# Performance work log

Hardware: AMD Instinct MI355X
Metric: run time of the kernel (lower is better)

The kernel has to match this reference:

```python
import jax, jax.numpy as jnp
import numpy as np

H = 16        # num_heads
E = 1024      # embed_size
OUT = 1024    # out_dim
TEMP = 1.0
EPS = 1e-20
LN_EPS = 1e-5


def setup_inputs() -> dict:
    key = jax.random.key(0)
    ks = jax.random.split(key, 16)
    B, S = 8, 4096
    s = 1.0 / np.sqrt(E)
    inp = {
        'x': jax.random.normal(ks[0], (B, S, E), dtype=jnp.float32),
        'gumbel_u': jax.random.uniform(ks[1], (B, H, S, 2), dtype=jnp.float32, minval=1e-6, maxval=1.0 - 1e-6),
        'query': jax.random.uniform(ks[2], (1, E), dtype=jnp.float32, minval=-s, maxval=s),  # xavier-ish
        'Wq': jax.random.uniform(ks[3], (E, E), jnp.float32, -s, s),
        'bq': jnp.zeros((E,), jnp.float32),
        'Wk': jax.random.uniform(ks[4], (E, E), jnp.float32, -s, s),
        'bk': jnp.zeros((E,), jnp.float32),
        'Wv': jax.random.uniform(ks[5], (E, E), jnp.float32, -s, s),
        'bv': jnp.zeros((E,), jnp.float32),
        'ln_g': jnp.ones((E,), jnp.float32),
        'ln_b': jnp.zeros((E,), jnp.float32),
        'W1': jax.random.uniform(ks[6], (4 * E, E), jnp.float32, -s, s),
        'b1': jnp.zeros((4 * E,), jnp.float32),
        'W2': jax.random.uniform(ks[7], (OUT, 4 * E), jnp.float32, -0.5 * s, 0.5 * s),
        'b2': jnp.zeros((OUT,), jnp.float32),
    }
    return inp


def reference(x, gumbel_u, query, Wq, bq, Wk, bk, Wv, bv, ln_g, ln_b, W1, b1, W2, b2):
    B, S, _ = x.shape
    dk = E // H
    # projections
    q = (query @ Wq.T + bq).reshape(H, dk)                      # [H, dk] (single query, broadcast over batch)
    k = (x @ Wk.T + bk).reshape(B, S, H, dk)                    # [B, S, H, dk]
    v = (x @ Wv.T + bv).reshape(B, S, H, dk)
    # single-query attention logits
    logits = jnp.einsum('hd,bshd->bhs', q, k) / np.sqrt(dk)     # [B, H, S]
    probs = jax.nn.softmax(logits, axis=-1)                     # [B, H, S]
    # gumbel-softmax hard mask over {keep=0-logit, drop/keep pair}
    edges = jnp.stack([jnp.zeros_like(logits), logits], axis=-1)  # [B, H, S, 2]
    g = -jnp.log(-jnp.log(gumbel_u + EPS) + EPS)
    y_soft = jax.nn.softmax((edges + g) / TEMP, axis=-1)
    idx = jnp.argmax(y_soft, axis=-1)
    y_hard = jax.nn.one_hot(idx, 2, dtype=y_soft.dtype)
    y = jax.lax.stop_gradient(y_hard - y_soft) + y_soft         # straight-through
    A = y[..., 1]                                               # [B, H, S]
    probs = A * probs
    # weighted sum of values; merge heads (seq_len of query is 1)
    hidden = jnp.einsum('bhs,bshd->bhd', probs, v).reshape(B, E)
    # layernorm
    mu = hidden.mean(axis=-1, keepdims=True)
    var = hidden.var(axis=-1, keepdims=True)
    hidden = (hidden - mu) / jnp.sqrt(var + LN_EPS) * ln_g + ln_b
    # MLP (dropout p=0 -> identity)
    out = jax.nn.relu(hidden @ W1.T + b1) @ W2.T + b2           # [B, OUT]
    masks = A.sum(axis=1)[:, None, :]                           # sum_heads=True -> [B, 1, S]
    attn = probs.sum(axis=1)[:, None, :]
    return out, masks, attn
```

## Files before the change

### kernel.cpp

```cpp
#include <hip/hip_runtime.h>
#include <hip/hip_bf16.h>
#include <math.h>

#define SS 4096
#define EE 1024
#define HH 16

typedef __bf16 bf16x8 __attribute__((ext_vector_type(8)));
typedef float  f32x4v __attribute__((ext_vector_type(4)));

#define OFF_QVEC 0L
#define OFF_QKB  1024L
#define OFF_QH   1040L
#define OFF_QL   9232L
#define OFF_SEC  17424L
#define OFF_SAC  50192L
#define OFF_WG   82960L
#define OFF_HID  607248L
#define OFF_T1   615440L
#define OFF_PX   648208L

__device__ __forceinline__ unsigned int pk_hi(float a, float b){
  return __builtin_amdgcn_perm(__float_as_uint(b), __float_as_uint(a), 0x07060302u);
}
__device__ __forceinline__ float lo_part(float f){
  return f - __uint_as_float(__float_as_uint(f) & 0xFFFF0000u);
}
__device__ __forceinline__ unsigned short f2bf_rn(float f){
  unsigned int u = __float_as_uint(f);
  return (unsigned short)((u + 0x7fffu + ((u >> 16) & 1u)) >> 16);
}
__device__ __forceinline__ f32x4v mfma16(bf16x8 a, bf16x8 b, f32x4v c){
  return __builtin_amdgcn_mfma_f32_16x16x32_bf16(a, b, c, 0, 0, 0);
}
__device__ __forceinline__ float waveRedSum(float v){
  #pragma unroll
  for (int m=1;m<64;m<<=1) v += __shfl_xor(v, m, 64);
  return v;
}
template<int NW>
__device__ __forceinline__ float blockRedSum(float v, volatile float* scr){
  v = waveRedSum(v);
  const int w = threadIdx.x >> 6;
  __syncthreads();
  if ((threadIdx.x & 63) == 0) scr[w] = v;
  __syncthreads();
  float r = 0.f;
  #pragma unroll
  for (int i=0;i<NW;i++) r += scr[i];
  return r;
}

__global__ __launch_bounds__(256) void k1(const float* __restrict__ query, const float* __restrict__ Wq,
                                          const float* __restrict__ bq, float* __restrict__ qvec,
                                          float* __restrict__ hid){
  const int wv = threadIdx.x >> 6, lane = threadIdx.x & 63;
  const int j = blockIdx.x * 4 + wv;
  float p = 0.f;
  #pragma unroll
  for (int i=0;i<4;i++){
    const int e = 4*lane + 256*i;
    const float4 q4 = *(const float4*)(query + e);
    const float4 w4 = *(const float4*)(Wq + (long)j*EE + e);
    p += q4.x*w4.x + q4.y*w4.y + q4.z*w4.z + q4.w*w4.w;
  }
  p = waveRedSum(p);
  if (lane == 0) qvec[j] = p + bq[j];
  if (blockIdx.x < 32) hid[blockIdx.x*256 + threadIdx.x] = 0.f;
}

__global__ __launch_bounds__(256) void k2(const float* __restrict__ Wk, const float* __restrict__ bk,
                                          const float* __restrict__ qvec,
                                          unsigned short* __restrict__ qh, unsigned short* __restrict__ ql,
                                          float* __restrict__ qkb){
  __shared__ float red[4][64];
  const int wv = threadIdx.x >> 6, lane = threadIdx.x & 63;
  const int h = blockIdx.y;
  const int e = blockIdx.x*64 + lane;
  float acc = 0.f;
  #pragma unroll
  for (int dd=0; dd<16; dd++){
    const int d = wv*16 + dd;
    acc += qvec[h*64+d] * Wk[(long)(h*64+d)*EE + e];
  }
  red[wv][lane] = acc;
  __syncthreads();
  if (wv == 0){
    const float s = red[0][lane] + red[1][lane] + red[2][lane] + red[3][lane];
    const unsigned int ub = __float_as_uint(s);
    qh[h*EE + e] = (unsigned short)(ub >> 16);
    const float lo = s - __uint_as_float(ub & 0xFFFF0000u);
    ql[h*EE + e] = (unsigned short)(__float_as_uint(lo) >> 16);
    if (blockIdx.x == 0){
      float p = qvec[h*64+lane] * bk[h*64+lane];
      p = waveRedSum(p);
      if (lane == 0) qkb[h] = p;
    }
  }
}

__global__ __launch_bounds__(256,2) void k3f(const float* __restrict__ x, const float* __restrict__ gum,
                                             const unsigned short* __restrict__ qh, const unsigned short* __restrict__ ql,
                                             const float* __restrict__ qkb,
                                             float* __restrict__ seC, float* __restrict__ saC,
                                             float* __restrict__ Wg, float* __restrict__ px,
                                             float* __restrict__ out){
  __shared__ unsigned short xsT[4][256*32];
  __shared__ float lg[4*16*17];
  __shared__ float wT[16][20];
  __shared__ float scrA[16*17], scrB[16*17];
  __shared__ float sQkb[16];
  const int t = threadIdx.x;
  const int wv = t >> 6, lane = t & 63;
  const int m16 = lane & 15, q = lane >> 4;
  const int blk = blockIdx.x, b = blockIdx.y;
  if (t < 16) sQkb[t] = qkb[t];
  unsigned short* xw = &xsT[wv][0];

  f32x4v P[16];
  #pragma unroll
  for (int i=0;i<16;i++){ P[i][0]=0.f; P[i][1]=0.f; P[i][2]=0.f; P[i][3]=0.f; }

  for (int ch=0; ch<4; ch++){
    const int c = blk*4 + ch;
    const long xbase = ((long)(b*SS + c*16))*EE;

    f32x4v a = {0.f,0.f,0.f,0.f};
    #pragma unroll
    for (int kt=0; kt<8; kt++){
      const int k = wv*256 + kt*32 + q*8;
      const float* xp = x + xbase + (long)m16*EE + k;
      const float4 f0 = *(const float4*)(xp);
      const float4 f1 = *(const float4*)(xp + 4);
      union { uint4 u; bf16x8 v; } xh, xl, bh, bl;
      xh.u.x = pk_hi(f0.x, f0.y); xh.u.y = pk_hi(f0.z, f0.w);
      xh.u.z = pk_hi(f1.x, f1.y); xh.u.w = pk_hi(f1.z, f1.w);
      xl.u.x = pk_hi(lo_part(f0.x), lo_part(f0.y)); xl.u.y = pk_hi(lo_part(f0.z), lo_part(f0.w));
      xl.u.z = pk_hi(lo_part(f1.x), lo_part(f1.y)); xl.u.w = pk_hi(lo_part(f1.z), lo_part(f1.w));
      bh.u = *(const uint4*)(qh + (long)m16*EE + k);
      bl.u = *(const uint4*)(ql + (long)m16*EE + k);
      a = mfma16(xh.v, bh.v, a);
      a = mfma16(xh.v, bl.v, a);
      a = mfma16(xl.v, bh.v, a);
      const int e0 = kt*32 + q*8;
      const unsigned hw[4] = {xh.u.x, xh.u.y, xh.u.z, xh.u.w};
      const unsigned lw[4] = {xl.u.x, xl.u.y, xl.u.z, xl.u.w};
      #pragma unroll
      for (int jj=0; jj<8; jj++){
        const unsigned sh = (jj & 1) * 16;
        xw[(e0+jj)*32 + m16]      = (unsigned short)(hw[jj>>1] >> sh);
        xw[(e0+jj)*32 + 16 + m16] = (unsigned short)(lw[jj>>1] >> sh);
      }
    }
    #pragma unroll
    for (int r=0;r<4;r++)
      lg[(wv*16 + q*4 + r)*17 + m16] = a[r];
    __syncthreads();

    {
      const int h = t & 15, s = t >> 4;
      const float dot = lg[(0*16+s)*17+h] + lg[(1*16+s)*17+h]
                      + lg[(2*16+s)*17+h] + lg[(3*16+s)*17+h];
      const float logit = (dot + sQkb[h]) * 0.125f;
      const long gi = ((long)(b*16 + h))*SS + c*16 + s;
      const float2 g2 = *(const float2*)(gum + 2*gi);
      const double gg0 = -log(-log((double)g2.x + 1e-20) + 1e-20);
      const double gg1 = -log(-log((double)g2.y + 1e-20) + 1e-20);
      const float e = expf(logit);
      const float wval = ((double)logit + gg1 > gg0) ? e : 0.f;
      wT[h][s] = wval;
      Wg[((long)b*SS + c*16 + s)*16 + h] = wval;
      scrA[s*17 + h] = e;
      scrB[s*17 + h] = wval;
    }
    __syncthreads();

    if (t < 16){
      float S = 0.f, SA = 0.f, cnt = 0.f;
      #pragma unroll
      for (int i=0;i<16;i++){ S += scrA[i*17 + t]; SA += scrB[i*17 + t]; }
      #pragma unroll
      for (int hh=0; hh<16; hh++) cnt += (scrB[t*17 + hh] > 0.f) ? 1.f : 0.f;
      seC[((long)(b*16 + t))*256 + c] = S;
      saC[((long)(b*16 + t))*256 + c] = SA;
      out[8192 + (long)b*SS + c*16 + t] = cnt;
    }

    {
      float wf[8];
      *(float4*)&wf[0] = *(const float4*)&wT[m16][(q & 1)*8];
      *(float4*)&wf[4] = *(const float4*)&wT[m16][(q & 1)*8 + 4];
      union { uint4 u; bf16x8 v; } B1, B2;
      B1.u.x = pk_hi(wf[0],wf[1]); B1.u.y = pk_hi(wf[2],wf[3]);
      B1.u.z = pk_hi(wf[4],wf[5]); B1.u.w = pk_hi(wf[6],wf[7]);
      B2.u.x = pk_hi(lo_part(wf[0]),lo_part(wf[1])); B2.u.y = pk_hi(lo_part(wf[2]),lo_part(wf[3]));
      B2.u.z = pk_hi(lo_part(wf[4]),lo_part(wf[5])); B2.u.w = pk_hi(lo_part(wf[6]),lo_part(wf[7]));
      #pragma unroll
      for (int et=0; et<16; et++){
        union { uint4 u; bf16x8 v; } A;
        A.u = *(const uint4*)(xw + (et*16 + m16)*32 + q*8);
        P[et] = mfma16(A.v, B1.v, P[et]);
        P[et] = mfma16(A.v, B2.v, P[et]);
      }
    }
  }

  const long pbase = (((long)(b*64 + blk))*16 + m16)*1024 + wv*256;
  #pragma unroll
  for (int et=0; et<16; et++){
    #pragma unroll
    for (int r=0;r<4;r++)
      px[pbase + et*16 + q*4 + r] = P[et][r];
  }
}

__global__ __launch_bounds__(256) void kb(const float* __restrict__ px, const float* __restrict__ Wg,
                                          const float* __restrict__ seC, const float* __restrict__ saC,
                                          const float* __restrict__ Wv, const float* __restrict__ bv,
                                          float* __restrict__ hid, float* __restrict__ out){
  __shared__ float s_red[16][17];
  __shared__ float sInv[16];
  __shared__ float scr1[4], scr2[4];
  __shared__ float xs[256];
  const int t = threadIdx.x;

  if (blockIdx.x < 32){
    const int b = blockIdx.x >> 2, sq = blockIdx.x & 3;
    { const int h = t >> 4, cl = t & 15;
      float se = 0.f;
      #pragma unroll
      for (int k=0;k<16;k++) se += seC[((long)(b*16+h))*256 + cl + 16*k];
      s_red[h][cl] = se;
    }
    __syncthreads();
    if (t < 16){
      float D = 0.f;
      #pragma unroll
      for (int i=0;i<16;i++) D += s_red[t][i];
      sInv[t] = 1.f / D;
    }
    __syncthreads();
    #pragma unroll
    for (int it=0; it<4; it++){
      const int s = sq*1024 + it*256 + t;
      const float* wr = Wg + ((long)b*SS + s)*16;
      float a = 0.f;
      #pragma unroll
      for (int h=0;h<16;h++) a += wr[h]*sInv[h];
      out[40960 + (long)b*SS + s] = a;
    }
    return;
  }

  const int idx = blockIdx.x - 32;
  const int b = idx >> 6, h = (idx >> 2) & 15, eq = idx & 3;
  const long rbase = ((long)(b*16 + h))*256;
  const float D    = blockRedSum<4>(seC[rbase + t], scr1);
  const float SA   = blockRedSum<4>(saC[rbase + t], scr2);
  const float invD = 1.f / D;
  const float psum = SA * invD;
  const float* pp = px + (((long)(b*64))*16 + h)*1024 + eq*256 + t;
  float xa = 0.f;
  #pragma unroll 8
  for (int seg=0; seg<64; seg++) xa += pp[(long)seg*16384];
  xs[t] = xa;
  __syncthreads();
  const int wv = t >> 6, lane = t & 63;
  const float4 xv = *(const float4*)(xs + 4*lane);
  #pragma unroll 4
  for (int jj=0; jj<16; jj++){
    const int j = h*64 + wv*16 + jj;
    const float4 w4 = *(const float4*)(Wv + (long)j*EE + eq*256 + 4*lane);
    float p = xv.x*w4.x + xv.y*w4.y + xv.z*w4.z + xv.w*w4.w;
    p = waveRedSum(p);
    if (lane == 0){
      float add = p * invD;
      if (eq == 0) add += psum * bv[j];
      atomicAdd(&hid[(long)b*EE + j], add);
    }
  }
}

__global__ __launch_bounds__(256) void k8f(const float* __restrict__ hid, const float* __restrict__ lng,
                                           const float* __restrict__ lnb, const float* __restrict__ W1,
                                           const float* __restrict__ b1, const float* __restrict__ b2,
                                           unsigned short* __restrict__ t1u, float* __restrict__ out){
  __shared__ unsigned short h2[16*1032];
  __shared__ float red[4*64*4];
  const int t = threadIdx.x;
  if (blockIdx.x < 32) out[blockIdx.x*256 + t] = b2[(blockIdx.x & 3)*256 + t];

  {
    const int r = t >> 5, ll = t & 31;
    float4 vv[8];
    float s1 = 0.f, s2 = 0.f;
    #pragma unroll
    for (int i=0;i<8;i++){
      vv[i] = *(const float4*)(hid + (long)r*1024 + ll*32 + i*4);
      s1 += vv[i].x + vv[i].y + vv[i].z + vv[i].w;
      s2 += vv[i].x*vv[i].x + vv[i].y*vv[i].y + vv[i].z*vv[i].z + vv[i].w*vv[i].w;
    }
    #pragma unroll
    for (int m=1;m<32;m<<=1){ s1 += __shfl_xor(s1, m, 32); s2 += __shfl_xor(s2, m, 32); }
    const float mu  = s1 * (1.f/1024.f);
    const float var = s2 * (1.f/1024.f) - mu*mu;
    const float rs  = rsqrtf(var + 1e-5f);
    #pragma unroll
    for (int i=0;i<8;i++){
      const int e = ll*32 + i*4;
      const float4 g4 = *(const float4*)(lng + e);
      const float4 b4 = *(const float4*)(lnb + e);
      uint2 pk;
      pk.x = (unsigned)f2bf_rn((vv[i].x-mu)*rs*g4.x + b4.x) | ((unsigned)f2bf_rn((vv[i].y-mu)*rs*g4.y + b4.y) << 16);
      pk.y = (unsigned)f2bf_rn((vv[i].z-mu)*rs*g4.z + b4.z) | ((unsigned)f2bf_rn((vv[i].w-mu)*rs*g4.w + b4.w) << 16);
      *(uint2*)(h2 + r*1032 + e) = pk;
      *(uint2*)(h2 + (8+r)*1032 + e) = make_uint2(0u, 0u);
    }
  }
  __syncthreads();

  const int wv = t >> 6, lane = t & 63;
  const int m16 = lane & 15, q = lane >> 4;
  const int j = blockIdx.x*16 + m16;
  f32x4v a = {0.f,0.f,0.f,0.f};
  #pragma unroll
  for (int kt=0; kt<8; kt++){
    const int k = wv*256 + kt*32 + q*8;
    union { uint4 u; bf16x8 v; } A, B;
    A.u = *(const uint4*)(h2 + m16*1032 + k);
    const float4 f0 = *(const float4*)(W1 + (long)j*EE + k);
    const float4 f1 = *(const float4*)(W1 + (long)j*EE + k + 4);
    B.u.x = pk_hi(f0.x,f0.y); B.u.y = pk_hi(f0.z,f0.w);
    B.u.z = pk_hi(f1.x,f1.y); B.u.w = pk_hi(f1.z,f1.w);
    a = mfma16(A.v, B.v, a);
  }
  #pragma unroll
  for (int r=0;r<4;r++) red[(wv*64 + lane)*4 + r] = a[r];
  __syncthreads();
  if (wv == 0){
    #pragma unroll
    for (int r=0;r<4;r++){
      const float s = red[(0*64+lane)*4+r] + red[(1*64+lane)*4+r]
                    + red[(2*64+lane)*4+r] + red[(3*64+lane)*4+r];
      const int row = q*4 + r;
      const float val = (row < 8) ? fmaxf(s + b1[j], 0.f) : 0.f;
      t1u[(long)row*4096 + j] = f2bf_rn(val);
    }
  }
}

__global__ __launch_bounds__(256) void k9a(const unsigned short* __restrict__ t1u, const float* __restrict__ W2,
                                           float* __restrict__ out){
  __shared__ float red[4*64*4];
  const int wv = threadIdx.x >> 6, lane = threadIdx.x & 63;
  const int m16 = lane & 15, q = lane >> 4;
  const int o = blockIdx.x*16 + m16;
  const int kbase = blockIdx.y*1024 + wv*256;
  f32x4v a = {0.f,0.f,0.f,0.f};
  #pragma unroll
  for (int kt=0; kt<8; kt++){
    const int k = kbase + kt*32 + q*8;
    union { uint4 u; bf16x8 v; } A, B;
    A.u = *(const uint4*)(t1u + (long)m16*4096 + k);
    const float4 f0 = *(const float4*)(W2 + (long)o*4096 + k);
    const float4 f1 = *(const float4*)(W2 + (long)o*4096 + k + 4);
    B.u.x = pk_hi(f0.x,f0.y); B.u.y = pk_hi(f0.z,f0.w);
    B.u.z = pk_hi(f1.x,f1.y); B.u.w = pk_hi(f1.z,f1.w);
    a = mfma16(A.v, B.v, a);
  }
  #pragma unroll
  for (int r=0;r<4;r++) red[(wv*64 + lane)*4 + r] = a[r];
  __syncthreads();
  if (wv == 0){
    #pragma unroll
    for (int r=0;r<4;r++){
      const int row = q*4 + r;
      if (row < 8){
        const float s = red[(0*64+lane)*4+r] + red[(1*64+lane)*4+r]
                      + red[(2*64+lane)*4+r] + red[(3*64+lane)*4+r];
        atomicAdd(out + row*1024 + o, s);
      }
    }
  }
}

extern "C" void kernel_launch(void* const* d_in, const int* in_sizes, int n_in,
                              void* d_out, int out_size, void* d_ws, size_t ws_size,
                              hipStream_t stream){
  const float* x    = (const float*)d_in[0];
  const float* gum  = (const float*)d_in[1];
  const float* query= (const float*)d_in[2];
  const float* Wq   = (const float*)d_in[3];
  const float* bq   = (const float*)d_in[4];
  const float* Wk   = (const float*)d_in[5];
  const float* bk   = (const float*)d_in[6];
  const float* Wv   = (const float*)d_in[7];
  const float* bv   = (const float*)d_in[8];
  const float* lng  = (const float*)d_in[9];
  const float* lnb  = (const float*)d_in[10];
  const float* W1   = (const float*)d_in[11];
  const float* b1   = (const float*)d_in[12];
  const float* W2   = (const float*)d_in[13];
  const float* b2   = (const float*)d_in[14];
  float* ws = (float*)d_ws;
  float* qvec = ws + OFF_QVEC;
  float* qkb  = ws + OFF_QKB;
  unsigned short* qh = (unsigned short*)(ws + OFF_QH);
  unsigned short* ql = (unsigned short*)(ws + OFF_QL);
  float* seC  = ws + OFF_SEC;
  float* saC  = ws + OFF_SAC;
  float* Wg   = ws + OFF_WG;
  float* hid  = ws + OFF_HID;
  unsigned short* t1u = (unsigned short*)(ws + OFF_T1);
  float* px   = ws + OFF_PX;
  float* out = (float*)d_out;

  k1  <<<256, 256, 0, stream>>>(query, Wq, bq, qvec, hid);
  k2  <<<dim3(16,16), 256, 0, stream>>>(Wk, bk, qvec, qh, ql, qkb);
  k3f <<<dim3(64,8), 256, 0, stream>>>(x, gum, qh, ql, qkb, seC, saC, Wg, px, out);
  kb  <<<544, 256, 0, stream>>>(px, Wg, seC, saC, Wv, bv, hid, out);
  k8f <<<256, 256, 0, stream>>>(hid, lng, lnb, W1, b1, b2, t1u, out);
  k9a <<<dim3(64,4), 256, 0, stream>>>(t1u, W2, out);
}
```

Baseline: 292.9 us.

## Fuse pipeline into cooperative persistent kernel with grid syncs and bf16 partials

Replaces six separate kernel launches with one cooperative kernel of 512 blocks whose phases are separated by grid-wide syncs, and keeps a multi-launch fallback. Idle blocks in the early phases precompute the double-precision Gumbel threshold differences, which takes the log work out of the attention phase. The per-block value partials are stored in bf16 instead of fp32 to halve that traffic, and the work split of the final GEMV and the attention-output pass is rebalanced. The risks are grid-sync overhead, lower occupancy from the large shared-memory footprint, and a small accuracy loss from bf16 partial sums.

```diff
diff --git a/kernel.cpp b/kernel.cpp
--- a/kernel.cpp
+++ b/kernel.cpp
@@ -1,6 +1,9 @@
 #include <hip/hip_runtime.h>
 #include <hip/hip_bf16.h>
+#include <hip/hip_cooperative_groups.h>
 #include <math.h>
+
+namespace cg = cooperative_groups;
 
 #define SS 4096
 #define EE 1024
@@ -18,8 +21,22 @@
 #define OFF_WG   82960L
 #define OFF_HID  607248L
 #define OFF_T1   615440L
-#define OFF_PX   648208L
-
+#define OFF_INVD 648208L
+#define OFF_PSUM 648336L
+#define OFF_PX   648464L
+#define OFF_GTH  4842768L
+
+struct MP {
+  const float *x, *gum, *query, *Wq, *bq, *Wk, *bk, *Wv, *bv, *lng, *lnb, *W1, *b1, *W2, *b2;
+  float *qvec, *qkb, *seC, *saC, *Wg, *hid, *invD, *psum;
+  double *gth;
+  unsigned short *qh, *ql, *t1u, *px;
+  float *out;
+};
+
+__device__ __forceinline__ float bf2f(unsigned int u){
+  union { unsigned int i; float f; } c; c.i = u << 16; return c.f;
+}
 __device__ __forceinline__ unsigned int pk_hi(float a, float b){
   return __builtin_amdgcn_perm(__float_as_uint(b), __float_as_uint(a), 0x07060302u);
 }
@@ -51,71 +68,85 @@
   return r;
 }
 
-__global__ __launch_bounds__(256) void k1(const float* __restrict__ query, const float* __restrict__ Wq,
-                                          const float* __restrict__ bq, float* __restrict__ qvec,
-                                          float* __restrict__ hid){
-  const int wv = threadIdx.x >> 6, lane = threadIdx.x & 63;
-  const int j = blockIdx.x * 4 + wv;
-  float p = 0.f;
-  #pragma unroll
-  for (int i=0;i<4;i++){
-    const int e = 4*lane + 256*i;
-    const float4 q4 = *(const float4*)(query + e);
-    const float4 w4 = *(const float4*)(Wq + (long)j*EE + e);
-    p += q4.x*w4.x + q4.y*w4.y + q4.z*w4.z + q4.w*w4.w;
-  }
-  p = waveRedSum(p);
-  if (lane == 0) qvec[j] = p + bq[j];
-  if (blockIdx.x < 32) hid[blockIdx.x*256 + threadIdx.x] = 0.f;
-}
-
-__global__ __launch_bounds__(256) void k2(const float* __restrict__ Wk, const float* __restrict__ bk,
-                                          const float* __restrict__ qvec,
-                                          unsigned short* __restrict__ qh, unsigned short* __restrict__ ql,
-                                          float* __restrict__ qkb){
-  __shared__ float red[4][64];
-  const int wv = threadIdx.x >> 6, lane = threadIdx.x & 63;
-  const int h = blockIdx.y;
-  const int e = blockIdx.x*64 + lane;
-  float acc = 0.f;
-  #pragma unroll
-  for (int dd=0; dd<16; dd++){
-    const int d = wv*16 + dd;
-    acc += qvec[h*64+d] * Wk[(long)(h*64+d)*EE + e];
-  }
-  red[wv][lane] = acc;
-  __syncthreads();
-  if (wv == 0){
-    const float s = red[0][lane] + red[1][lane] + red[2][lane] + red[3][lane];
-    const unsigned int ub = __float_as_uint(s);
-    qh[h*EE + e] = (unsigned short)(ub >> 16);
-    const float lo = s - __uint_as_float(ub & 0xFFFF0000u);
-    ql[h*EE + e] = (unsigned short)(__float_as_uint(lo) >> 16);
-    if (blockIdx.x == 0){
-      float p = qvec[h*64+lane] * bk[h*64+lane];
-      p = waveRedSum(p);
-      if (lane == 0) qkb[h] = p;
-    }
-  }
-}
-
-__global__ __launch_bounds__(256,2) void k3f(const float* __restrict__ x, const float* __restrict__ gum,
-                                             const unsigned short* __restrict__ qh, const unsigned short* __restrict__ ql,
-                                             const float* __restrict__ qkb,
-                                             float* __restrict__ seC, float* __restrict__ saC,
-                                             float* __restrict__ Wg, float* __restrict__ px,
-                                             float* __restrict__ out){
-  __shared__ unsigned short xsT[4][256*32];
-  __shared__ float lg[4*16*17];
-  __shared__ float wT[16][20];
-  __shared__ float scrA[16*17], scrB[16*17];
-  __shared__ float sQkb[16];
-  const int t = threadIdx.x;
+__device__ __forceinline__ double gdiff(float u0, float u1){
+  const double g0 = -log(-log((double)u0 + 1e-20) + 1e-20);
+  const double g1 = -log(-log((double)u1 + 1e-20) + 1e-20);
+  return g0 - g1;
+}
+__device__ __forceinline__ void ph_gth(const MP& p, long i0){
+  const float4 a4 = *(const float4*)(p.gum + 2*i0);
+  const float4 b4 = *(const float4*)(p.gum + 2*i0 + 4);
+  p.gth[i0+0] = gdiff(a4.x, a4.y);
+  p.gth[i0+1] = gdiff(a4.z, a4.w);
+  p.gth[i0+2] = gdiff(b4.x, b4.y);
+  p.gth[i0+3] = gdiff(b4.z, b4.w);
+}
+
+__device__ void phase0(const MP& p, int bid, int t){
+  const int wv = t >> 6, lane = t & 63;
+  if (bid < 256){
+    const int j = bid*4 + wv;
+    float acc = 0.f;
+    #pragma unroll
+    for (int i=0;i<4;i++){
+      const int e = 4*lane + 256*i;
+      const float4 q4 = *(const float4*)(p.query + e);
+      const float4 w4 = *(const float4*)(p.Wq + (long)j*EE + e);
+      acc += q4.x*w4.x + q4.y*w4.y + q4.z*w4.z + q4.w*w4.w;
+    }
+    acc = waveRedSum(acc);
+    if (lane == 0) p.qvec[j] = acc + p.bq[j];
+  } else {
+    const int ib = bid - 256;
+    if (ib < 32) p.hid[ib*256 + t] = 0.f;
+    else if (ib < 64) p.out[(ib-32)*256 + t] = p.b2[((ib-32)&3)*256 + t];
+    ph_gth(p, (long)ib*1024 + t*4);
+  }
+}
+
+__device__ void phase1(const MP& p, int bid, int t, char* SMc){
+  const int wv = t >> 6, lane = t & 63;
+  if (bid < 256){
+    float* red = (float*)SMc;
+    const int h = bid >> 4;
+    const int e = (bid & 15)*64 + lane;
+    float acc = 0.f;
+    #pragma unroll
+    for (int dd=0; dd<16; dd++){
+      const int d = wv*16 + dd;
+      acc += p.qvec[h*64+d] * p.Wk[(long)(h*64+d)*EE + e];
+    }
+    red[wv*64 + lane] = acc;
+    __syncthreads();
+    if (wv == 0){
+      const float s = red[lane] + red[64+lane] + red[128+lane] + red[192+lane];
+      const unsigned int ub = __float_as_uint(s);
+      p.qh[h*EE + e] = (unsigned short)(ub >> 16);
+      const float lo = s - __uint_as_float(ub & 0xFFFF0000u);
+      p.ql[h*EE + e] = (unsigned short)(__float_as_uint(lo) >> 16);
+      if ((bid & 15) == 0){
+        float pr = p.qvec[h*64+lane] * p.bk[h*64+lane];
+        pr = waveRedSum(pr);
+        if (lane == 0) p.qkb[h] = pr;
+      }
+    }
+  } else {
+    ph_gth(p, 262144L + (long)(bid-256)*1024 + t*4);
+  }
+}
+
+__device__ void phase2(const MP& p, int bid, int t, char* SMc){
+  unsigned short* xsT = (unsigned short*)SMc;
+  float* lg   = (float*)(SMc + 65536);
+  float* wT   = (float*)(SMc + 69888);
+  float* scrA = (float*)(SMc + 71168);
+  float* scrB = (float*)(SMc + 72256);
+  float* sQkb = (float*)(SMc + 73344);
   const int wv = t >> 6, lane = t & 63;
   const int m16 = lane & 15, q = lane >> 4;
-  const int blk = blockIdx.x, b = blockIdx.y;
-  if (t < 16) sQkb[t] = qkb[t];
-  unsigned short* xw = &xsT[wv][0];
+  const int blk = bid & 63, b = bid >> 6;
+  if (t < 16) sQkb[t] = p.qkb[t];
+  unsigned short* xw = xsT + wv*8192;
 
   f32x4v P[16];
   #pragma unroll
@@ -129,7 +160,7 @@
     #pragma unroll
     for (int kt=0; kt<8; kt++){
       const int k = wv*256 + kt*32 + q*8;
-      const float* xp = x + xbase + (long)m16*EE + k;
+      const float* xp = p.x + xbase + (long)m16*EE + k;
       const float4 f0 = *(const float4*)(xp);
       const float4 f1 = *(const float4*)(xp + 4);
       union { uint4 u; bf16x8 v; } xh, xl, bh, bl;
@@ -137,8 +168,8 @@
       xh.u.z = pk_hi(f1.x, f1.y); xh.u.w = pk_hi(f1.z, f1.w);
       xl.u.x = pk_hi(lo_part(f0.x), lo_part(f0.y)); xl.u.y = pk_hi(lo_part(f0.z), lo_part(f0.w));
       xl.u.z = pk_hi(lo_part(f1.x), lo_part(f1.y)); xl.u.w = pk_hi(lo_part(f1.z), lo_part(f1.w));
-      bh.u = *(const uint4*)(qh + (long)m16*EE + k);
-      bl.u = *(const uint4*)(ql + (long)m16*EE + k);
+      bh.u = *(const uint4*)(p.qh + (long)m16*EE + k);
+      bl.u = *(const uint4*)(p.ql + (long)m16*EE + k);
       a = mfma16(xh.v, bh.v, a);
       a = mfma16(xh.v, bl.v, a);
       a = mfma16(xl.v, bh.v, a);
@@ -159,17 +190,14 @@
 
     {
       const int h = t & 15, s = t >> 4;
-      const float dot = lg[(0*16+s)*17+h] + lg[(1*16+s)*17+h]
-                      + lg[(2*16+s)*17+h] + lg[(3*16+s)*17+h];
+      const float dot = lg[s*17+h] + lg[(16+s)*17+h] + lg[(32+s)*17+h] + lg[(48+s)*17+h];
       const float logit = (dot + sQkb[h]) * 0.125f;
       const long gi = ((long)(b*16 + h))*SS + c*16 + s;
-      const float2 g2 = *(const float2*)(gum + 2*gi);
-      const double gg0 = -log(-log((double)g2.x + 1e-20) + 1e-20);
-      const double gg1 = -log(-log((double)g2.y + 1e-20) + 1e-20);
+      const double gthd = p.gth[gi];
       const float e = expf(logit);
-      const float wval = ((double)logit + gg1 > gg0) ? e : 0.f;
-      wT[h][s] = wval;
-      Wg[((long)b*SS + c*16 + s)*16 + h] = wval;
+      const float wval = ((double)logit > gthd) ? e : 0.f;
+      wT[h*20 + s] = wval;
+      p.Wg[((long)b*SS + c*16 + s)*16 + h] = wval;
       scrA[s*17 + h] = e;
       scrB[s*17 + h] = wval;
     }
@@ -181,15 +209,15 @@
       for (int i=0;i<16;i++){ S += scrA[i*17 + t]; SA += scrB[i*17 + t]; }
       #pragma unroll
       for (int hh=0; hh<16; hh++) cnt += (scrB[t*17 + hh] > 0.f) ? 1.f : 0.f;
-      seC[((long)(b*16 + t))*256 + c] = S;
-      saC[((long)(b*16 + t))*256 + c] = SA;
-      out[8192 + (long)b*SS + c*16 + t] = cnt;
+      p.seC[((long)(b*16 + t))*256 + c] = S;
+      p.saC[((long)(b*16 + t))*256 + c] = SA;
+      p.out[8192 + (long)b*SS + c*16 + t] = cnt;
     }
 
     {
       float wf[8];
-      *(float4*)&wf[0] = *(const float4*)&wT[m16][(q & 1)*8];
-      *(float4*)&wf[4] = *(const float4*)&wT[m16][(q & 1)*8 + 4];
+      *(float4*)&wf[0] = *(const float4*)&wT[m16*20 + (q & 1)*8];
+      *(float4*)&wf[4] = *(const float4*)&wT[m16*20 + (q & 1)*8 + 4];
       union { uint4 u; bf16x8 v; } B1, B2;
       B1.u.x = pk_hi(wf[0],wf[1]); B1.u.y = pk_hi(wf[2],wf[3]);
       B1.u.z = pk_hi(wf[4],wf[5]); B1.u.w = pk_hi(wf[6],wf[7]);
@@ -208,61 +236,28 @@
   const long pbase = (((long)(b*64 + blk))*16 + m16)*1024 + wv*256;
   #pragma unroll
   for (int et=0; et<16; et++){
-    #pragma unroll
-    for (int r=0;r<4;r++)
-      px[pbase + et*16 + q*4 + r] = P[et][r];
-  }
-}
-
-__global__ __launch_bounds__(256) void kb(const float* __restrict__ px, const float* __restrict__ Wg,
-                                          const float* __restrict__ seC, const float* __restrict__ saC,
-                                          const float* __restrict__ Wv, const float* __restrict__ bv,
-                                          float* __restrict__ hid, float* __restrict__ out){
-  __shared__ float s_red[16][17];
-  __shared__ float sInv[16];
-  __shared__ float scr1[4], scr2[4];
-  __shared__ float xs[256];
-  const int t = threadIdx.x;
-
-  if (blockIdx.x < 32){
-    const int b = blockIdx.x >> 2, sq = blockIdx.x & 3;
-    { const int h = t >> 4, cl = t & 15;
-      float se = 0.f;
-      #pragma unroll
-      for (int k=0;k<16;k++) se += seC[((long)(b*16+h))*256 + cl + 16*k];
-      s_red[h][cl] = se;
-    }
-    __syncthreads();
-    if (t < 16){
-      float D = 0.f;
-      #pragma unroll
-      for (int i=0;i<16;i++) D += s_red[t][i];
-      sInv[t] = 1.f / D;
-    }
-    __syncthreads();
-    #pragma unroll
-    for (int it=0; it<4; it++){
-      const int s = sq*1024 + it*256 + t;
-      const float* wr = Wg + ((long)b*SS + s)*16;
-      float a = 0.f;
-      #pragma unroll
-      for (int h=0;h<16;h++) a += wr[h]*sInv[h];
-      out[40960 + (long)b*SS + s] = a;
-    }
-    return;
-  }
-
-  const int idx = blockIdx.x - 32;
-  const int b = idx >> 6, h = (idx >> 2) & 15, eq = idx & 3;
+    uint2 pk2;
+    pk2.x = (unsigned)f2bf_rn(P[et][0]) | ((unsigned)f2bf_rn(P[et][1]) << 16);
+    pk2.y = (unsigned)f2bf_rn(P[et][2]) | ((unsigned)f2bf_rn(P[et][3]) << 16);
+    *(uint2*)(p.px + pbase + et*16 + q*4) = pk2;
+  }
+}
+
+__device__ void phase3(const MP& p, int bid, int t, char* SMc){
+  float* scr1 = (float*)SMc;
+  float* scr2 = scr1 + 16;
+  float* xs   = scr1 + 32;
+  const int b = bid >> 6, h = (bid >> 2) & 15, eq = bid & 3;
   const long rbase = ((long)(b*16 + h))*256;
-  const float D    = blockRedSum<4>(seC[rbase + t], scr1);
-  const float SA   = blockRedSum<4>(saC[rbase + t], scr2);
+  const float D    = blockRedSum<4>(p.seC[rbase + t], scr1);
+  const float SA   = blockRedSum<4>(p.saC[rbase + t], scr2);
   const float invD = 1.f / D;
   const float psum = SA * invD;
-  const float* pp = px + (((long)(b*64))*16 + h)*1024 + eq*256 + t;
+  if (eq == 0 && t == 0){ p.invD[b*16+h] = invD; p.psum[b*16+h] = psum; }
+  const unsigned short* pp = p.px + (((long)(b*64))*16 + h)*1024 + eq*256 + t;
   float xa = 0.f;
   #pragma unroll 8
-  for (int seg=0; seg<64; seg++) xa += pp[(long)seg*16384];
+  for (int seg=0; seg<64; seg++) xa += bf2f((unsigned)pp[(long)seg*16384]);
   xs[t] = xa;
   __syncthreads();
   const int wv = t >> 6, lane = t & 63;
@@ -270,66 +265,107 @@
   #pragma unroll 4
   for (int jj=0; jj<16; jj++){
     const int j = h*64 + wv*16 + jj;
-    const float4 w4 = *(const float4*)(Wv + (long)j*EE + eq*256 + 4*lane);
-    float p = xv.x*w4.x + xv.y*w4.y + xv.z*w4.z + xv.w*w4.w;
-    p = waveRedSum(p);
+    const float4 w4 = *(const float4*)(p.Wv + (long)j*EE + eq*256 + 4*lane);
+    float pr = xv.x*w4.x + xv.y*w4.y + xv.z*w4.z + xv.w*w4.w;
+    pr = waveRedSum(pr);
     if (lane == 0){
-      float add = p * invD;
-      if (eq == 0) add += psum * bv[j];
-      atomicAdd(&hid[(long)b*EE + j], add);
-    }
-  }
-}
-
-__global__ __launch_bounds__(256) void k8f(const float* __restrict__ hid, const float* __restrict__ lng,
-                                           const float* __restrict__ lnb, const float* __restrict__ W1,
-                                           const float* __restrict__ b1, const float* __restrict__ b2,
-                                           unsigned short* __restrict__ t1u, float* __restrict__ out){
-  __shared__ unsigned short h2[16*1032];
-  __shared__ float red[4*64*4];
-  const int t = threadIdx.x;
-  if (blockIdx.x < 32) out[blockIdx.x*256 + t] = b2[(blockIdx.x & 3)*256 + t];
-
-  {
-    const int r = t >> 5, ll = t & 31;
-    float4 vv[8];
-    float s1 = 0.f, s2 = 0.f;
-    #pragma unroll
-    for (int i=0;i<8;i++){
-      vv[i] = *(const float4*)(hid + (long)r*1024 + ll*32 + i*4);
-      s1 += vv[i].x + vv[i].y + vv[i].z + vv[i].w;
-      s2 += vv[i].x*vv[i].x + vv[i].y*vv[i].y + vv[i].z*vv[i].z + vv[i].w*vv[i].w;
-    }
-    #pragma unroll
-    for (int m=1;m<32;m<<=1){ s1 += __shfl_xor(s1, m, 32); s2 += __shfl_xor(s2, m, 32); }
-    const float mu  = s1 * (1.f/1024.f);
-    const float var = s2 * (1.f/1024.f) - mu*mu;
-    const float rs  = rsqrtf(var + 1e-5f);
-    #pragma unroll
-    for (int i=0;i<8;i++){
-      const int e = ll*32 + i*4;
-      const float4 g4 = *(const float4*)(lng + e);
-      const float4 b4 = *(const float4*)(lnb + e);
-      uint2 pk;
-      pk.x = (unsigned)f2bf_rn((vv[i].x-mu)*rs*g4.x + b4.x) | ((unsigned)f2bf_rn((vv[i].y-mu)*rs*g4.y + b4.y) << 16);
-      pk.y = (unsigned)f2bf_rn((vv[i].z-mu)*rs*g4.z + b4.z) | ((unsigned)f2bf_rn((vv[i].w-mu)*rs*g4.w + b4.w) << 16);
-      *(uint2*)(h2 + r*1032 + e) = pk;
-      *(uint2*)(h2 + (8+r)*1032 + e) = make_uint2(0u, 0u);
-    }
-  }
-  __syncthreads();
-
+      float add = pr * invD;
+      if (eq == 0) add += psum * p.bv[j];
+      atomicAdd(&p.hid[(long)b*EE + j], add);
+    }
+  }
+}
+
+__device__ void phase4(const MP& p, int bid, int t, char* SMc){
+  const int wv = t >> 6, lane = t & 63;
+  if (bid < 256){
+    unsigned short* h2 = (unsigned short*)SMc;
+    float* red = (float*)(SMc + 33024);
+    {
+      const int r = t >> 5, ll = t & 31;
+      float4 vv[8];
+      float s1 = 0.f, s2 = 0.f;
+      #pragma unroll
+      for (int i=0;i<8;i++){
+        vv[i] = *(const float4*)(p.hid + (long)r*1024 + ll*32 + i*4);
+        s1 += vv[i].x + vv[i].y + vv[i].z + vv[i].w;
+        s2 += vv[i].x*vv[i].x + vv[i].y*vv[i].y + vv[i].z*vv[i].z + vv[i].w*vv[i].w;
+      }
+      #pragma unroll
+      for (int m=1;m<32;m<<=1){ s1 += __shfl_xor(s1, m, 32); s2 += __shfl_xor(s2, m, 32); }
+      const float mu  = s1 * (1.f/1024.f);
+      const float var = s2 * (1.f/1024.f) - mu*mu;
+      const float rs  = rsqrtf(var + 1e-5f);
+      #pragma unroll
+      for (int i=0;i<8;i++){
+        const int e = ll*32 + i*4;
+        const float4 g4 = *(const float4*)(p.lng + e);
+        const float4 b4 = *(const float4*)(p.lnb + e);
+        uint2 pk;
+        pk.x = (unsigned)f2bf_rn((vv[i].x-mu)*rs*g4.x + b4.x) | ((unsigned)f2bf_rn((vv[i].y-mu)*rs*g4.y + b4.y) << 16);
+        pk.y = (unsigned)f2bf_rn((vv[i].z-mu)*rs*g4.z + b4.z) | ((unsigned)f2bf_rn((vv[i].w-mu)*rs*g4.w + b4.w) << 16);
+        *(uint2*)(h2 + r*1032 + e) = pk;
+        *(uint2*)(h2 + (8+r)*1032 + e) = make_uint2(0u, 0u);
+      }
+    }
+    __syncthreads();
+    const int m16 = lane & 15, q = lane >> 4;
+    const int j = bid*16 + m16;
+    f32x4v a = {0.f,0.f,0.f,0.f};
+    #pragma unroll
+    for (int kt=0; kt<8; kt++){
+      const int k = wv*256 + kt*32 + q*8;
+      union { uint4 u; bf16x8 v; } A, B;
+      A.u = *(const uint4*)(h2 + m16*1032 + k);
+      const float4 f0 = *(const float4*)(p.W1 + (long)j*EE + k);
+      const float4 f1 = *(const float4*)(p.W1 + (long)j*EE + k + 4);
+      B.u.x = pk_hi(f0.x,f0.y); B.u.y = pk_hi(f0.z,f0.w);
+      B.u.z = pk_hi(f1.x,f1.y); B.u.w = pk_hi(f1.z,f1.w);
+      a = mfma16(A.v, B.v, a);
+    }
+    #pragma unroll
+    for (int r=0;r<4;r++) red[(wv*64 + lane)*4 + r] = a[r];
+    __syncthreads();
+    if (wv == 0){
+      #pragma unroll
+      for (int r=0;r<4;r++){
+        const float s = red[lane*4+r] + red[(64+lane)*4+r] + red[(128+lane)*4+r] + red[(192+lane)*4+r];
+        const int row = q*4 + r;
+        const float val = (row < 8) ? fmaxf(s + p.b1[j], 0.f) : 0.f;
+        p.t1u[(long)row*4096 + j] = f2bf_rn(val);
+      }
+    }
+  } else {
+    float* sInv = (float*)SMc;
+    const int idx2 = bid - 256;
+    const int b = idx2 >> 5, seg = idx2 & 31;
+    if (t < 16) sInv[t] = p.invD[b*16 + t];
+    __syncthreads();
+    if (t < 128){
+      const int s = seg*128 + t;
+      const float* wr = p.Wg + ((long)b*SS + s)*16;
+      float a = 0.f;
+      #pragma unroll
+      for (int h=0;h<16;h++) a += wr[h]*sInv[h];
+      p.out[40960 + (long)b*SS + s] = a;
+    }
+  }
+}
+
+__device__ void phase5(const MP& p, int bid, int t, char* SMc){
+  float* red = (float*)SMc;
   const int wv = t >> 6, lane = t & 63;
   const int m16 = lane & 15, q = lane >> 4;
-  const int j = blockIdx.x*16 + m16;
+  const int o = (bid & 63)*16 + m16;
+  const int kbase = (bid >> 6)*512 + wv*128;
   f32x4v a = {0.f,0.f,0.f,0.f};
   #pragma unroll
-  for (int kt=0; kt<8; kt++){
-    const int k = wv*256 + kt*32 + q*8;
+  for (int kt=0; kt<4; kt++){
+    const int k = kbase + kt*32 + q*8;
     union { uint4 u; bf16x8 v; } A, B;
-    A.u = *(const uint4*)(h2 + m16*1032 + k);
-    const float4 f0 = *(const float4*)(W1 + (long)j*EE + k);
-    const float4 f1 = *(const float4*)(W1 + (long)j*EE + k + 4);
+    A.u = *(const uint4*)(p.t1u + (long)m16*4096 + k);
+    const float4 f0 = *(const float4*)(p.W2 + (long)o*4096 + k);
+    const float4 f1 = *(const float4*)(p.W2 + (long)o*4096 + k + 4);
     B.u.x = pk_hi(f0.x,f0.y); B.u.y = pk_hi(f0.z,f0.w);
     B.u.z = pk_hi(f1.x,f1.y); B.u.w = pk_hi(f1.z,f1.w);
     a = mfma16(A.v, B.v, a);
@@ -340,85 +376,78 @@
   if (wv == 0){
     #pragma unroll
     for (int r=0;r<4;r++){
-      const float s = red[(0*64+lane)*4+r] + red[(1*64+lane)*4+r]
-                    + red[(2*64+lane)*4+r] + red[(3*64+lane)*4+r];
-      const int row = q*4 + r;
-      const float val = (row < 8) ? fmaxf(s + b1[j], 0.f) : 0.f;
-      t1u[(long)row*4096 + j] = f2bf_rn(val);
-    }
-  }
-}
-
-__global__ __launch_bounds__(256) void k9a(const unsigned short* __restrict__ t1u, const float* __restrict__ W2,
-                                           float* __restrict__ out){
-  __shared__ float red[4*64*4];
-  const int wv = threadIdx.x >> 6, lane = threadIdx.x & 63;
-  const int m16 = lane & 15, q = lane >> 4;
-  const int o = blockIdx.x*16 + m16;
-  const int kbase = blockIdx.y*1024 + wv*256;
-  f32x4v a = {0.f,0.f,0.f,0.f};
-  #pragma unroll
-  for (int kt=0; kt<8; kt++){
-    const int k = kbase + kt*32 + q*8;
-    union { uint4 u; bf16x8 v; } A, B;
-    A.u = *(const uint4*)(t1u + (long)m16*4096 + k);
-    const float4 f0 = *(const float4*)(W2 + (long)o*4096 + k);
-    const float4 f1 = *(const float4*)(W2 + (long)o*4096 + k + 4);
-    B.u.x = pk_hi(f0.x,f0.y); B.u.y = pk_hi(f0.z,f0.w);
-    B.u.z = pk_hi(f1.x,f1.y); B.u.w = pk_hi(f1.z,f1.w);
-    a = mfma16(A.v, B.v, a);
-  }
-  #pragma unroll
-  for (int r=0;r<4;r++) red[(wv*64 + lane)*4 + r] = a[r];
-  __syncthreads();
-  if (wv == 0){
-    #pragma unroll
-    for (int r=0;r<4;r++){
       const int row = q*4 + r;
       if (row < 8){
-        const float s = red[(0*64+lane)*4+r] + red[(1*64+lane)*4+r]
-                      + red[(2*64+lane)*4+r] + red[(3*64+lane)*4+r];
-        atomicAdd(out + row*1024 + o, s);
-      }
-    }
-  }
-}
+        const float s = red[lane*4+r] + red[(64+lane)*4+r] + red[(128+lane)*4+r] + red[(192+lane)*4+r];
+        atomicAdd(p.out + row*1024 + o, s);
+      }
+    }
+  }
+}
+
+__global__ __launch_bounds__(256,2) void mega(MP p){
+  __shared__ __align__(16) char SMc[73408];
+  cg::grid_group g = cg::this_grid();
+  const int t = threadIdx.x, bid = blockIdx.x;
+  phase0(p, bid, t);        g.sync();
+  phase1(p, bid, t, SMc);   g.sync();
+  phase2(p, bid, t, SMc);   g.sync();
+  phase3(p, bid, t, SMc);   g.sync();
+  phase4(p, bid, t, SMc);   g.sync();
+  phase5(p, bid, t, SMc);
+}
+
+__global__ __launch_bounds__(256,2) void kp0(MP p){ phase0(p, blockIdx.x, threadIdx.x); }
+__global__ __launch_bounds__(256,2) void kp1(MP p){ __shared__ __align__(16) char SMc[73408]; phase1(p, blockIdx.x, threadIdx.x, SMc); }
+__global__ __launch_bounds__(256,2) void kp2(MP p){ __shared__ __align__(16) char SMc[73408]; phase2(p, blockIdx.x, threadIdx.x, SMc); }
+__global__ __launch_bounds__(256,2) void kp3(MP p){ __shared__ __align__(16) char SMc[73408]; phase3(p, blockIdx.x, threadIdx.x, SMc); }
+__global__ __launch_bounds__(256,2) void kp4(MP p){ __shared__ __align__(16) char SMc[73408]; phase4(p, blockIdx.x, threadIdx.x, SMc); }
+__global__ __launch_bounds__(256,2) void kp5(MP p){ __shared__ __align__(16) char SMc[73408]; phase5(p, blockIdx.x, threadIdx.x, SMc); }
 
 extern "C" void kernel_launch(void* const* d_in, const int* in_sizes, int n_in,
                               void* d_out, int out_size, void* d_ws, size_t ws_size,
                               hipStream_t stream){
-  const float* x    = (const float*)d_in[0];
-  const float* gum  = (const float*)d_in[1];
-  const float* query= (const float*)d_in[2];
-  const float* Wq   = (const float*)d_in[3];
-  const float* bq   = (const float*)d_in[4];
-  const float* Wk   = (const float*)d_in[5];
-  const float* bk   = (const float*)d_in[6];
-  const float* Wv   = (const float*)d_in[7];
-  const float* bv   = (const float*)d_in[8];
-  const float* lng  = (const float*)d_in[9];
-  const float* lnb  = (const float*)d_in[10];
-  const float* W1   = (const float*)d_in[11];
-  const float* b1   = (const float*)d_in[12];
-  const float* W2   = (const float*)d_in[13];
-  const float* b2   = (const float*)d_in[14];
   float* ws = (float*)d_ws;
-  float* qvec = ws + OFF_QVEC;
-  float* qkb  = ws + OFF_QKB;
-  unsigned short* qh = (unsigned short*)(ws + OFF_QH);
-  unsigned short* ql = (unsigned short*)(ws + OFF_QL);
-  float* seC  = ws + OFF_SEC;
-  float* saC  = ws + OFF_SAC;
-  float* Wg   = ws + OFF_WG;
-  float* hid  = ws + OFF_HID;
-  unsigned short* t1u = (unsigned short*)(ws + OFF_T1);
-  float* px   = ws + OFF_PX;
-  float* out = (float*)d_out;
-
-  k1  <<<256, 256, 0, stream>>>(query, Wq, bq, qvec, hid);
-  k2  <<<dim3(16,16), 256, 0, stream>>>(Wk, bk, qvec, qh, ql, qkb);
-  k3f <<<dim3(64,8), 256, 0, stream>>>(x, gum, qh, ql, qkb, seC, saC, Wg, px, out);
-  kb  <<<544, 256, 0, stream>>>(px, Wg, seC, saC, Wv, bv, hid, out);
-  k8f <<<256, 256, 0, stream>>>(hid, lng, lnb, W1, b1, b2, t1u, out);
-  k9a <<<dim3(64,4), 256, 0, stream>>>(t1u, W2, out);
-}
+  MP p;
+  p.x    = (const float*)d_in[0];
+  p.gum  = (const float*)d_in[1];
+  p.query= (const float*)d_in[2];
+  p.Wq   = (const float*)d_in[3];
+  p.bq   = (const float*)d_in[4];
+  p.Wk   = (const float*)d_in[5];
+  p.bk   = (const float*)d_in[6];
+  p.Wv   = (const float*)d_in[7];
+  p.bv   = (const float*)d_in[8];
+  p.lng  = (const float*)d_in[9];
+  p.lnb  = (const float*)d_in[10];
+  p.W1   = (const float*)d_in[11];
+  p.b1   = (const float*)d_in[12];
+  p.W2   = (const float*)d_in[13];
+  p.b2   = (const float*)d_in[14];
+  p.qvec = ws + OFF_QVEC;
+  p.qkb  = ws + OFF_QKB;
+  p.qh   = (unsigned short*)(ws + OFF_QH);
+  p.ql   = (unsigned short*)(ws + OFF_QL);
+  p.seC  = ws + OFF_SEC;
+  p.saC  = ws + OFF_SAC;
+  p.Wg   = ws + OFF_WG;
+  p.hid  = ws + OFF_HID;
+  p.t1u  = (unsigned short*)(ws + OFF_T1);
+  p.invD = ws + OFF_INVD;
+  p.psum = ws + OFF_PSUM;
+  p.px   = (unsigned short*)(ws + OFF_PX);
+  p.gth  = (double*)(ws + OFF_GTH);
+  p.out  = (float*)d_out;
+
+  void* args[] = { (void*)&p };
+  hipError_t err = hipLaunchCooperativeKernel((const void*)mega, dim3(512), dim3(256), args, 0, stream);
+  if (err != hipSuccess){
+    (void)hipGetLastError();
+    kp0<<<512, 256, 0, stream>>>(p);
+    kp1<<<512, 256, 0, stream>>>(p);
+    kp2<<<512, 256, 0, stream>>>(p);
+    kp3<<<512, 256, 0, stream>>>(p);
+    kp4<<<512, 256, 0, stream>>>(p);
+    kp5<<<512, 256, 0, stream>>>(p);
+  }
+}
```

Result: slower. 617.4 us (+110.8%).

## Precompute gumbel thresholds in k1, pack px to bf16, repack x tile stores

Applied to the files above, without the earlier changes.

Moves the double-precision gumbel log-log computation out of the main attention kernel into extra blocks of the first kernel, which write a per-element double threshold that k3f compares against. Partial value sums px are stored as bf16 instead of fp32, halving that intermediate traffic. Shared-memory transposed x stores are merged into 32-bit writes via perm, and the output bias initialization moves to k1. This adds a B*H*S double buffer round-trip and loses precision in px.

```diff
diff --git a/kernel.cpp b/kernel.cpp
--- a/kernel.cpp
+++ b/kernel.cpp
@@ -19,7 +19,11 @@
 #define OFF_HID  607248L
 #define OFF_T1   615440L
 #define OFF_PX   648208L
-
+#define OFF_GTH  4842512L
+
+__device__ __forceinline__ float bf2f(unsigned int u){
+  union { unsigned int i; float f; } c; c.i = u << 16; return c.f;
+}
 __device__ __forceinline__ unsigned int pk_hi(float a, float b){
   return __builtin_amdgcn_perm(__float_as_uint(b), __float_as_uint(a), 0x07060302u);
 }
@@ -50,23 +54,44 @@
   for (int i=0;i<NW;i++) r += scr[i];
   return r;
 }
+__device__ __forceinline__ double gdiff(float u0, float u1){
+  const double g0 = -log(-log((double)u0 + 1e-20) + 1e-20);
+  const double g1 = -log(-log((double)u1 + 1e-20) + 1e-20);
+  return g0 - g1;
+}
 
 __global__ __launch_bounds__(256) void k1(const float* __restrict__ query, const float* __restrict__ Wq,
-                                          const float* __restrict__ bq, float* __restrict__ qvec,
-                                          float* __restrict__ hid){
-  const int wv = threadIdx.x >> 6, lane = threadIdx.x & 63;
-  const int j = blockIdx.x * 4 + wv;
-  float p = 0.f;
-  #pragma unroll
-  for (int i=0;i<4;i++){
-    const int e = 4*lane + 256*i;
-    const float4 q4 = *(const float4*)(query + e);
-    const float4 w4 = *(const float4*)(Wq + (long)j*EE + e);
-    p += q4.x*w4.x + q4.y*w4.y + q4.z*w4.z + q4.w*w4.w;
-  }
-  p = waveRedSum(p);
-  if (lane == 0) qvec[j] = p + bq[j];
-  if (blockIdx.x < 32) hid[blockIdx.x*256 + threadIdx.x] = 0.f;
+                                          const float* __restrict__ bq, const float* __restrict__ gum,
+                                          const float* __restrict__ b2,
+                                          float* __restrict__ qvec, double* __restrict__ gth,
+                                          float* __restrict__ hid, float* __restrict__ out){
+  const int t = threadIdx.x;
+  const int wv = t >> 6, lane = t & 63;
+  const int bid = blockIdx.x;
+  if (bid < 256){
+    const int j = bid*4 + wv;
+    float p = 0.f;
+    #pragma unroll
+    for (int i=0;i<4;i++){
+      const int e = 4*lane + 256*i;
+      const float4 q4 = *(const float4*)(query + e);
+      const float4 w4 = *(const float4*)(Wq + (long)j*EE + e);
+      p += q4.x*w4.x + q4.y*w4.y + q4.z*w4.z + q4.w*w4.w;
+    }
+    p = waveRedSum(p);
+    if (lane == 0) qvec[j] = p + bq[j];
+  } else {
+    const int ib = bid - 256;
+    if (ib < 32) hid[ib*256 + t] = 0.f;
+    else if (ib < 64) out[(ib-32)*256 + t] = b2[((ib-32)&3)*256 + t];
+    const long i0 = (long)ib*1024 + t*4;
+    const float4 a4 = *(const float4*)(gum + 2*i0);
+    const float4 b4 = *(const float4*)(gum + 2*i0 + 4);
+    gth[i0+0] = gdiff(a4.x, a4.y);
+    gth[i0+1] = gdiff(a4.z, a4.w);
+    gth[i0+2] = gdiff(b4.x, b4.y);
+    gth[i0+3] = gdiff(b4.z, b4.w);
+  }
 }
 
 __global__ __launch_bounds__(256) void k2(const float* __restrict__ Wk, const float* __restrict__ bk,
@@ -99,13 +124,13 @@
   }
 }
 
-__global__ __launch_bounds__(256,2) void k3f(const float* __restrict__ x, const float* __restrict__ gum,
+__global__ __launch_bounds__(256,2) void k3f(const float* __restrict__ x, const double* __restrict__ gth,
                                              const unsigned short* __restrict__ qh, const unsigned short* __restrict__ ql,
                                              const float* __restrict__ qkb,
                                              float* __restrict__ seC, float* __restrict__ saC,
-                                             float* __restrict__ Wg, float* __restrict__ px,
+                                             float* __restrict__ Wg, unsigned short* __restrict__ px,
                                              float* __restrict__ out){
-  __shared__ unsigned short xsT[4][256*32];
+  __shared__ unsigned int xsT[4][256*16];
   __shared__ float lg[4*16*17];
   __shared__ float wT[16][20];
   __shared__ float scrA[16*17], scrB[16*17];
@@ -115,7 +140,8 @@
   const int m16 = lane & 15, q = lane >> 4;
   const int blk = blockIdx.x, b = blockIdx.y;
   if (t < 16) sQkb[t] = qkb[t];
-  unsigned short* xw = &xsT[wv][0];
+  unsigned int* xw32 = &xsT[wv][0];
+  const unsigned short* xw16 = (const unsigned short*)xw32;
 
   f32x4v P[16];
   #pragma unroll
@@ -142,14 +168,14 @@
       a = mfma16(xh.v, bh.v, a);
       a = mfma16(xh.v, bl.v, a);
       a = mfma16(xl.v, bh.v, a);
-      const int e0 = kt*32 + q*8;
       const unsigned hw[4] = {xh.u.x, xh.u.y, xh.u.z, xh.u.w};
       const unsigned lw[4] = {xl.u.x, xl.u.y, xl.u.z, xl.u.w};
+      const int rowbase = (kt*32 + q*8)*16 + m16;
       #pragma unroll
       for (int jj=0; jj<8; jj++){
-        const unsigned sh = (jj & 1) * 16;
-        xw[(e0+jj)*32 + m16]      = (unsigned short)(hw[jj>>1] >> sh);
-        xw[(e0+jj)*32 + 16 + m16] = (unsigned short)(lw[jj>>1] >> sh);
+        const unsigned val = __builtin_amdgcn_perm(lw[jj>>1], hw[jj>>1],
+                                                   (jj & 1) ? 0x07060302u : 0x05040100u);
+        xw32[rowbase + jj*16] = val;
       }
     }
     #pragma unroll
@@ -159,15 +185,12 @@
 
     {
       const int h = t & 15, s = t >> 4;
-      const float dot = lg[(0*16+s)*17+h] + lg[(1*16+s)*17+h]
-                      + lg[(2*16+s)*17+h] + lg[(3*16+s)*17+h];
+      const float dot = lg[s*17+h] + lg[(16+s)*17+h] + lg[(32+s)*17+h] + lg[(48+s)*17+h];
       const float logit = (dot + sQkb[h]) * 0.125f;
       const long gi = ((long)(b*16 + h))*SS + c*16 + s;
-      const float2 g2 = *(const float2*)(gum + 2*gi);
-      const double gg0 = -log(-log((double)g2.x + 1e-20) + 1e-20);
-      const double gg1 = -log(-log((double)g2.y + 1e-20) + 1e-20);
+      const double gthd = gth[gi];
       const float e = expf(logit);
-      const float wval = ((double)logit + gg1 > gg0) ? e : 0.f;
+      const float wval = ((double)logit > gthd) ? e : 0.f;
       wT[h][s] = wval;
       Wg[((long)b*SS + c*16 + s)*16 + h] = wval;
       scrA[s*17 + h] = e;
@@ -187,18 +210,17 @@
     }
 
     {
-      float wf[8];
-      *(float4*)&wf[0] = *(const float4*)&wT[m16][(q & 1)*8];
-      *(float4*)&wf[4] = *(const float4*)&wT[m16][(q & 1)*8 + 4];
+      const float4 w4 = *(const float4*)&wT[m16][q*4];
       union { uint4 u; bf16x8 v; } B1, B2;
-      B1.u.x = pk_hi(wf[0],wf[1]); B1.u.y = pk_hi(wf[2],wf[3]);
-      B1.u.z = pk_hi(wf[4],wf[5]); B1.u.w = pk_hi(wf[6],wf[7]);
-      B2.u.x = pk_hi(lo_part(wf[0]),lo_part(wf[1])); B2.u.y = pk_hi(lo_part(wf[2]),lo_part(wf[3]));
-      B2.u.z = pk_hi(lo_part(wf[4]),lo_part(wf[5])); B2.u.w = pk_hi(lo_part(wf[6]),lo_part(wf[7]));
+      B1.u.x = pk_hi(w4.x, w4.x); B1.u.y = pk_hi(w4.y, w4.y);
+      B1.u.z = pk_hi(w4.z, w4.z); B1.u.w = pk_hi(w4.w, w4.w);
+      const float l0 = lo_part(w4.x), l1 = lo_part(w4.y), l2 = lo_part(w4.z), l3 = lo_part(w4.w);
+      B2.u.x = pk_hi(l0, l0); B2.u.y = pk_hi(l1, l1);
+      B2.u.z = pk_hi(l2, l2); B2.u.w = pk_hi(l3, l3);
       #pragma unroll
       for (int et=0; et<16; et++){
         union { uint4 u; bf16x8 v; } A;
-        A.u = *(const uint4*)(xw + (et*16 + m16)*32 + q*8);
+        A.u = *(const uint4*)(xw16 + (et*16 + m16)*32 + q*8);
         P[et] = mfma16(A.v, B1.v, P[et]);
         P[et] = mfma16(A.v, B2.v, P[et]);
       }
@@ -208,13 +230,14 @@
   const long pbase = (((long)(b*64 + blk))*16 + m16)*1024 + wv*256;
   #pragma unroll
   for (int et=0; et<16; et++){
-    #pragma unroll
-    for (int r=0;r<4;r++)
-      px[pbase + et*16 + q*4 + r] = P[et][r];
-  }
-}
-
-__global__ __launch_bounds__(256) void kb(const float* __restrict__ px, const float* __restrict__ Wg,
+    uint2 pk2;
+    pk2.x = (unsigned)f2bf_rn(P[et][0]) | ((unsigned)f2bf_rn(P[et][1]) << 16);
+    pk2.y = (unsigned)f2bf_rn(P[et][2]) | ((unsigned)f2bf_rn(P[et][3]) << 16);
+    *(uint2*)(px + pbase + et*16 + q*4) = pk2;
+  }
+}
+
+__global__ __launch_bounds__(256) void kb(const unsigned short* __restrict__ px, const float* __restrict__ Wg,
                                           const float* __restrict__ seC, const float* __restrict__ saC,
                                           const float* __restrict__ Wv, const float* __restrict__ bv,
                                           float* __restrict__ hid, float* __restrict__ out){
@@ -259,10 +282,10 @@
   const float SA   = blockRedSum<4>(saC[rbase + t], scr2);
   const float invD = 1.f / D;
   const float psum = SA * invD;
-  const float* pp = px + (((long)(b*64))*16 + h)*1024 + eq*256 + t;
+  const unsigned short* pp = px + (((long)(b*64))*16 + h)*1024 + eq*256 + t;
   float xa = 0.f;
   #pragma unroll 8
-  for (int seg=0; seg<64; seg++) xa += pp[(long)seg*16384];
+  for (int seg=0; seg<64; seg++) xa += bf2f((unsigned)pp[(long)seg*16384]);
   xs[t] = xa;
   __syncthreads();
   const int wv = t >> 6, lane = t & 63;
@@ -271,10 +294,10 @@
   for (int jj=0; jj<16; jj++){
     const int j = h*64 + wv*16 + jj;
     const float4 w4 = *(const float4*)(Wv + (long)j*EE + eq*256 + 4*lane);
-    float p = xv.x*w4.x + xv.y*w4.y + xv.z*w4.z + xv.w*w4.w;
-    p = waveRedSum(p);
+    float pr = xv.x*w4.x + xv.y*w4.y + xv.z*w4.z + xv.w*w4.w;
+    pr = waveRedSum(pr);
     if (lane == 0){
-      float add = p * invD;
+      float add = pr * invD;
       if (eq == 0) add += psum * bv[j];
       atomicAdd(&hid[(long)b*EE + j], add);
     }
@@ -283,13 +306,11 @@
 
 __global__ __launch_bounds__(256) void k8f(const float* __restrict__ hid, const float* __restrict__ lng,
                                            const float* __restrict__ lnb, const float* __restrict__ W1,
-                                           const float* __restrict__ b1, const float* __restrict__ b2,
-                                           unsigned short* __restrict__ t1u, float* __restrict__ out){
+                                           const float* __restrict__ b1,
+                                           unsigned short* __restrict__ t1u){
   __shared__ unsigned short h2[16*1032];
   __shared__ float red[4*64*4];
   const int t = threadIdx.x;
-  if (blockIdx.x < 32) out[blockIdx.x*256 + t] = b2[(blockIdx.x & 3)*256 + t];
-
   {
     const int r = t >> 5, ll = t & 31;
     float4 vv[8];
@@ -318,7 +339,6 @@
     }
   }
   __syncthreads();
-
   const int wv = t >> 6, lane = t & 63;
   const int m16 = lane & 15, q = lane >> 4;
   const int j = blockIdx.x*16 + m16;
@@ -340,8 +360,7 @@
   if (wv == 0){
     #pragma unroll
     for (int r=0;r<4;r++){
-      const float s = red[(0*64+lane)*4+r] + red[(1*64+lane)*4+r]
-                    + red[(2*64+lane)*4+r] + red[(3*64+lane)*4+r];
+      const float s = red[lane*4+r] + red[(64+lane)*4+r] + red[(128+lane)*4+r] + red[(192+lane)*4+r];
       const int row = q*4 + r;
       const float val = (row < 8) ? fmaxf(s + b1[j], 0.f) : 0.f;
       t1u[(long)row*4096 + j] = f2bf_rn(val);
@@ -376,8 +395,7 @@
     for (int r=0;r<4;r++){
       const int row = q*4 + r;
       if (row < 8){
-        const float s = red[(0*64+lane)*4+r] + red[(1*64+lane)*4+r]
-                      + red[(2*64+lane)*4+r] + red[(3*64+lane)*4+r];
+        const float s = red[lane*4+r] + red[(64+lane)*4+r] + red[(128+lane)*4+r] + red[(192+lane)*4+r];
         atomicAdd(out + row*1024 + o, s);
       }
     }
@@ -412,13 +430,14 @@
   float* Wg   = ws + OFF_WG;
   float* hid  = ws + OFF_HID;
   unsigned short* t1u = (unsigned short*)(ws + OFF_T1);
-  float* px   = ws + OFF_PX;
+  unsigned short* px  = (unsigned short*)(ws + OFF_PX);
+  double* gth = (double*)(ws + OFF_GTH);
   float* out = (float*)d_out;
 
-  k1  <<<256, 256, 0, stream>>>(query, Wq, bq, qvec, hid);
+  k1  <<<768, 256, 0, stream>>>(query, Wq, bq, gum, b2, qvec, gth, hid, out);
   k2  <<<dim3(16,16), 256, 0, stream>>>(Wk, bk, qvec, qh, ql, qkb);
-  k3f <<<dim3(64,8), 256, 0, stream>>>(x, gum, qh, ql, qkb, seC, saC, Wg, px, out);
+  k3f <<<dim3(64,8), 256, 0, stream>>>(x, gth, qh, ql, qkb, seC, saC, Wg, px, out);
   kb  <<<544, 256, 0, stream>>>(px, Wg, seC, saC, Wv, bv, hid, out);
-  k8f <<<256, 256, 0, stream>>>(hid, lng, lnb, W1, b1, b2, t1u, out);
+  k8f <<<256, 256, 0, stream>>>(hid, lng, lnb, W1, b1, t1u);
   k9a <<<dim3(64,4), 256, 0, stream>>>(t1u, W2, out);
 }
```

Measured after the change: 291.1 us. About the same (-0.6%).
